# Optimization experiments

Hardware: AMD Instinct MI355X
Metric: run time of the kernel (lower is better)

## Reference

```python
import jax, jax.numpy as jnp
import numpy as np

G = 1024        # graphs in batch
NPG = 64        # nodes per graph
EPG = 256       # edges per graph
N = G * NPG     # 65536 total nodes
E = G * EPG     # 262144 total edges
IN_CH = 768
CH = 128
RATIO = 0.5
K = int(RATIO * EPG)  # edges reserved as 'causal' per graph


def setup_inputs() -> dict:
    key = jax.random.key(0)
    ks = jax.random.split(key, 10)
    w = lambda k, shape, fan: (jax.random.normal(k, shape, jnp.float32) / np.float32(np.sqrt(fan)))
    x = jax.random.normal(ks[0], (N, IN_CH), jnp.float32)
    # per-graph random edges, offset into the global node index space
    ei = jax.random.randint(ks[1], (2, G, EPG), 0, NPG)
    edge_index = (ei + (jnp.arange(G) * NPG)[None, :, None]).reshape(2, -1).astype(jnp.int32)
    edge_attr = jax.random.uniform(ks[2], (E,), jnp.float32)  # positive edge weights
    batch = jnp.repeat(jnp.arange(G, dtype=jnp.int32), NPG)
    return dict(
        x=x, edge_index=edge_index, edge_attr=edge_attr, batch=batch,
        W1=w(ks[3], (IN_CH, CH), IN_CH), V1=w(ks[4], (IN_CH, CH), IN_CH), b1=jnp.zeros((CH,), jnp.float32),
        W2=w(ks[5], (CH, CH), CH),       V2=w(ks[6], (CH, CH), CH),       b2=jnp.zeros((CH,), jnp.float32),
        mw1=w(ks[7], (2 * CH, 4 * CH), 2 * CH), mb1=jnp.zeros((4 * CH,), jnp.float32),
        mw2=w(ks[8], (4 * CH, 1), 4 * CH),      mb2=jnp.zeros((1,), jnp.float32),
    )


def reference(x, edge_index, edge_attr, batch, W1, V1, b1, W2, V2, b2, mw1, mb1, mw2, mb2):
    row, col = edge_index[0], edge_index[1]
    ew = edge_attr.reshape(-1)

    # gcn_norm (symmetric, no self loops), as used inside ARMAConv
    deg = jnp.zeros((N,), x.dtype).at[col].add(ew)
    dis = jnp.where(deg > 0, jax.lax.rsqrt(jnp.where(deg > 0, deg, 1.0)), 0.0)
    norm = dis[row] * ew * dis[col]  # [E]

    def arma(h, W, V, b):
        # ARMAConv, num_stacks=1, num_layers=1: ReLU(A_hat (h W) + h V + b)
        m = h @ W                                            # [N, C]
        agg = jnp.zeros((N, W.shape[1]), h.dtype).at[col].add(norm[:, None] * m[row])
        return jax.nn.relu(agg + h @ V + b)

    x1 = jax.nn.relu(arma(x, W1, V1, b1))  # outer F.relu (idempotent after internal ReLU)
    x2 = arma(x1, W2, V2, b2)              # [N, CH]

    # edge-gather MLP -> scalar score per edge
    edge_rep = jnp.concatenate([x2[row], x2[col]], axis=-1)          # [E, 2C]
    pred_edge_weight = (jax.nn.relu(edge_rep @ mw1 + mb1) @ mw2 + mb2).reshape(-1)  # [E]

    # per-graph top-k split (batched replacement of the numpy argpartition loop)
    wg = pred_edge_weight.reshape(G, EPG)
    order = jnp.argsort(-wg, axis=1)                                  # descending
    base = (jnp.arange(G) * EPG)[:, None]
    cid = (base + order[:, :K]).reshape(-1)   # causal (reserved) edge ids
    did = (base + order[:, K:]).reshape(-1)   # conf (dropped) edge ids

    causal = (x2, edge_index[:, cid], edge_attr[cid], pred_edge_weight[cid], batch)
    conf = (x2, edge_index[:, did], edge_attr[did], -pred_edge_weight[did], batch)
    return (*causal, *conf, pred_edge_weight)
```

## Files before the change

kernel.cpp:

```cpp
#include <hip/hip_runtime.h>
#include <hip/hip_bf16.h>
#include <stdint.h>

#define G_    1024
#define NPG   64
#define EPG   256
#define N_    (G_*NPG)
#define E_    (G_*EPG)
#define IN_CH 768
#define CH    128
#define KSEL  128
#define HID   512

#define NCH  (N_*CH)
#define GK   (G_*KSEL)
#define OFF0 0
#define OFF1 (OFF0 + NCH)
#define OFF2 (OFF1 + 2*GK)
#define OFF3 (OFF2 + GK)
#define OFF4 (OFF3 + GK)
#define OFF5 (OFF4 + N_)
#define OFF6 (OFF5 + NCH)
#define OFF7 (OFF6 + 2*GK)
#define OFF8 (OFF7 + GK)
#define OFF9 (OFF8 + GK)
#define OFF10 (OFF9 + N_)

typedef unsigned short u16;
typedef unsigned int   u32;
typedef __attribute__((ext_vector_type(8))) short bf16x8;
typedef __attribute__((ext_vector_type(4))) float f32x4;

__device__ __forceinline__ u16 f2bf(float x) {
    union { float f; u32 u; } v; v.f = x;
    u32 r = v.u + 0x7fffu + ((v.u >> 16) & 1u);
    return (u16)(r >> 16);
}
__device__ __forceinline__ float bf2f(u32 h) {
    union { u32 u; float f; } v; v.u = h << 16; return v.f;
}
__device__ __forceinline__ u16 bfc(float x) {
    __hip_bfloat16 h = __float2bfloat16(x);
    return *reinterpret_cast<u16*>(&h);
}

__global__ void k_concat(const float* __restrict__ W1, const float* __restrict__ V1,
                         const float* __restrict__ W2, const float* __restrict__ V2,
                         const float* __restrict__ mw1,
                         u16* __restrict__ WV1t, u16* __restrict__ WV2t,
                         u16* __restrict__ Mwt) {
    int i = blockIdx.x * 256 + threadIdx.x;
    if (i < 256 * IN_CH) {
        int c = i / IN_CH, r = i - c * IN_CH;
        WV1t[i] = f2bf(c < CH ? W1[r*CH + c] : V1[r*CH + (c - CH)]);
    }
    if (i < 256 * CH) {
        int c = i >> 7, r = i & 127;
        WV2t[i] = f2bf(c < CH ? W2[r*CH + c] : V2[r*CH + (c - CH)]);
    }
    if (i < 1024 * CH) {
        int c = i >> 7, r = i & 127;
        Mwt[i] = f2bf(c < HID ? mw1[r*HID + c] : mw1[(CH + r)*HID + (c - HID)]);
    }
}

__global__ __launch_bounds__(256) void k_gemm1(const float* __restrict__ Ap,
        const u16* __restrict__ Bt, u16* __restrict__ Cp) {
    __shared__ float As[2][128 * 32];
    const int t = threadIdx.x;
    const int lane = t & 63, w = t >> 6;
    const int wr = (w >> 1) << 6, wc = (w & 1) << 6;
    const size_t bm = (size_t)blockIdx.x * 128;
    const size_t bn = (size_t)blockIdx.y * 128;
    const int r16 = lane & 15, kq = lane >> 4;

    int cid[4], grow[4], gcol[4];
    #pragma unroll
    for (int i = 0; i < 4; ++i) {
        int c = i * 256 + t;
        cid[i] = c;
        int row = c >> 3, sl = c & 7;
        grow[i] = row;
        gcol[i] = (sl ^ (row & 7)) * 4;
    }

    f32x4 acc[4][4];
    #pragma unroll
    for (int m = 0; m < 4; ++m)
        #pragma unroll
        for (int n = 0; n < 4; ++n)
            acc[m][n] = (f32x4){0.f, 0.f, 0.f, 0.f};

    #define STAGE(buf, k0)                                                      \
        do {                                                                    \
            _Pragma("unroll")                                                   \
            for (int i = 0; i < 4; ++i) {                                       \
                const float* src = Ap + (bm + grow[i]) * (size_t)IN_CH + (k0) + gcol[i]; \
                __builtin_amdgcn_global_load_lds(                               \
                    (const __attribute__((address_space(1))) void*)src,         \
                    (__attribute__((address_space(3))) void*)&As[buf][cid[i] * 4], \
                    16, 0, 0);                                                  \
            }                                                                   \
        } while (0)

    #define LOADB(bv, k0)                                                       \
        do {                                                                    \
            _Pragma("unroll")                                                   \
            for (int n = 0; n < 4; ++n)                                         \
                bv[n] = *(const bf16x8*)(Bt + (bn + wc + n * 16 + r16) * (size_t)IN_CH + (k0) + kq * 8); \
        } while (0)

    STAGE(0, 0);
    bf16x8 bc[4];
    LOADB(bc, 0);
    __syncthreads();

    const int nk = IN_CH / 32;
    int buf = 0;
    for (int ki = 0; ki < nk; ++ki) {
        bf16x8 bnx[4];
        if (ki + 1 < nk) {
            STAGE(buf ^ 1, (ki + 1) * 32);
            LOADB(bnx, (ki + 1) * 32);
        }
        bf16x8 a[4];
        #pragma unroll
        for (int m = 0; m < 4; ++m) {
            int row = wr + m * 16 + r16;
            int xr = row & 7;
            const float* base = &As[buf][row * 32];
            float4 q0 = *(const float4*)(base + (((2 * kq)     ^ xr) * 4));
            float4 q1 = *(const float4*)(base + (((2 * kq + 1) ^ xr) * 4));
            union { bf16x8 v; u16 s[8]; } pk;
            pk.s[0] = bfc(q0.x); pk.s[1] = bfc(q0.y); pk.s[2] = bfc(q0.z); pk.s[3] = bfc(q0.w);
            pk.s[4] = bfc(q1.x); pk.s[5] = bfc(q1.y); pk.s[6] = bfc(q1.z); pk.s[7] = bfc(q1.w);
            a[m] = pk.v;
        }
        #pragma unroll
        for (int m = 0; m < 4; ++m)
            #pragma unroll
            for (int n = 0; n < 4; ++n)
                acc[m][n] = __builtin_amdgcn_mfma_f32_16x16x32_bf16(a[m], bc[n], acc[m][n], 0, 0, 0);
        if (ki + 1 < nk) {
            #pragma unroll
            for (int n = 0; n < 4; ++n) bc[n] = bnx[n];
        }
        __syncthreads();
        buf ^= 1;
    }
    #undef STAGE
    #undef LOADB

    #pragma unroll
    for (int m = 0; m < 4; ++m)
        #pragma unroll
        for (int j = 0; j < 4; ++j) {
            size_t row = bm + wr + m * 16 + kq * 4 + j;
            #pragma unroll
            for (int n = 0; n < 4; ++n) {
                size_t col = bn + wc + n * 16 + r16;
                Cp[row * 256 + col] = f2bf(acc[m][n][j]);
            }
        }
}

__global__ __launch_bounds__(512, 4) void k_graph(const u16* __restrict__ B1b,
        const u16* __restrict__ WV2t, const u16* __restrict__ Mwt,
        const int* __restrict__ ei,
        const float* __restrict__ b1, const float* __restrict__ b2,
        const float* __restrict__ mb1, const float* __restrict__ mw2,
        const float* __restrict__ mb2, const float* __restrict__ ea,
        float* __restrict__ out) {
    __shared__ char Lds[71168];
    float* A_s   = (float*)(Lds + 0);
    float* key   = (float*)(Lds + 0);
    u16*   x1s   = (u16*)(Lds + 16640);
    u16*   x2s   = (u16*)(Lds + 16640);
    u16*   Ms    = (u16*)(Lds + 34048);
    u16*   MVs   = (u16*)(Lds + 34048);
    u16*   PQc   = (u16*)(Lds + 34048);
    float* mw2s  = (float*)(Lds + 68864);
    float* deg_s = (float*)(Lds + 70912);

    const int g = blockIdx.x, t = threadIdx.x;
    const int lane = t & 63, w = t >> 6;
    const int r16 = lane & 15, kq = lane >> 4;
    const size_t nbase = (size_t)g * 64;
    union bfr { bf16x8 v; u16 s[8]; };

    if (t < 128) *(float4*)&mw2s[t * 4] = *(const float4*)&mw2[t * 4];
    for (int i = t; i < 64 * 65; i += 512) A_s[i] = 0.f;
    if (t < 64) deg_s[t] = 0.f;
    for (int i = t; i < 64 * 32; i += 512) {
        int row = i >> 5, c4 = (i & 31) << 2;
        *(uint2*)&Ms[row * 136 + c4] = *(const uint2*)(B1b + (nbase + row) * 256 + c4);
    }
    int rfull = 0, cfull = 0, er = 0, ec = 0; float eav = 0.f;
    if (t < 256) {
        int e = g * 256 + t;
        rfull = ei[e]; cfull = ei[E_ + e];
        er = rfull & 63; ec = cfull & 63;
        eav = ea[e];
    }
    __syncthreads();
    if (t < 256) atomicAdd(&deg_s[ec], eav);
    __syncthreads();
    if (t < 256) {
        float dr = deg_s[er], dc = deg_s[ec];
        float fr = dr > 0.f ? 1.0f / sqrtf(dr) : 0.f;
        float fc = dc > 0.f ? 1.0f / sqrtf(dc) : 0.f;
        atomicAdd(&A_s[er * 65 + ec], fr * eav * fc);
    }
    __syncthreads();

    {
        const int n0 = w * 16;
        f32x4 acc[4];
        #pragma unroll
        for (int mt = 0; mt < 4; ++mt) acc[mt] = (f32x4){0.f, 0.f, 0.f, 0.f};
        #pragma unroll
        for (int ks = 0; ks < 2; ++ks) {
            bfr a[4], b;
            #pragma unroll
            for (int mt = 0; mt < 4; ++mt)
                #pragma unroll
                for (int i = 0; i < 8; ++i)
                    a[mt].s[i] = f2bf(A_s[(ks*32 + kq*8 + i) * 65 + mt*16 + r16]);
            #pragma unroll
            for (int i = 0; i < 8; ++i)
                b.s[i] = Ms[(ks*32 + kq*8 + i) * 136 + n0 + r16];
            #pragma unroll
            for (int mt = 0; mt < 4; ++mt)
                acc[mt] = __builtin_amdgcn_mfma_f32_16x16x32_bf16(a[mt].v, b.v, acc[mt], 0, 0, 0);
        }
        const int ch = w * 16 + r16;
        __syncthreads();
        #pragma unroll
        for (int mt = 0; mt < 4; ++mt)
            #pragma unroll
            for (int j = 0; j < 4; ++j) {
                int c = mt * 16 + kq * 4 + j;
                float v = bf2f(B1b[(nbase + c) * 256 + 128 + ch]) + b1[ch];
                x1s[c * 136 + ch] = f2bf(fmaxf(acc[mt][j] + v, 0.f));
            }
    }
    __syncthreads();

    {
        const int wc2 = w * 32;
        f32x4 acc[4][2];
        #pragma unroll
        for (int mt = 0; mt < 4; ++mt)
            #pragma unroll
            for (int n = 0; n < 2; ++n) acc[mt][n] = (f32x4){0.f, 0.f, 0.f, 0.f};
        #pragma unroll
        for (int ks = 0; ks < 4; ++ks) {
            bf16x8 a[4], b[2];
            #pragma unroll
            for (int mt = 0; mt < 4; ++mt)
                a[mt] = *(const bf16x8*)&x1s[(mt*16 + r16) * 136 + ks*32 + kq*8];
            #pragma unroll
            for (int n = 0; n < 2; ++n)
                b[n] = *(const bf16x8*)(WV2t + (size_t)(wc2 + n*16 + r16) * 128 + ks*32 + kq*8);
            #pragma unroll
            for (int mt = 0; mt < 4; ++mt)
                #pragma unroll
                for (int n = 0; n < 2; ++n)
                    acc[mt][n] = __builtin_amdgcn_mfma_f32_16x16x32_bf16(a[mt], b[n], acc[mt][n], 0, 0, 0);
        }
        #pragma unroll
        for (int mt = 0; mt < 4; ++mt)
            #pragma unroll
            for (int j = 0; j < 4; ++j) {
                int row = mt * 16 + kq * 4 + j;
                #pragma unroll
                for (int n = 0; n < 2; ++n)
                    MVs[row * 272 + wc2 + n*16 + r16] = f2bf(acc[mt][n][j]);
            }
    }
    __syncthreads();

    {
        const int n0 = w * 16;
        f32x4 acc[4];
        #pragma unroll
        for (int mt = 0; mt < 4; ++mt) acc[mt] = (f32x4){0.f, 0.f, 0.f, 0.f};
        #pragma unroll
        for (int ks = 0; ks < 2; ++ks) {
            bfr a[4], b;
            #pragma unroll
            for (int mt = 0; mt < 4; ++mt)
                #pragma unroll
                for (int i = 0; i < 8; ++i)
                    a[mt].s[i] = f2bf(A_s[(ks*32 + kq*8 + i) * 65 + mt*16 + r16]);
            #pragma unroll
            for (int i = 0; i < 8; ++i)
                b.s[i] = MVs[(ks*32 + kq*8 + i) * 272 + n0 + r16];
            #pragma unroll
            for (int mt = 0; mt < 4; ++mt)
                acc[mt] = __builtin_amdgcn_mfma_f32_16x16x32_bf16(a[mt].v, b.v, acc[mt], 0, 0, 0);
        }
        const int ch = w * 16 + r16;
        #pragma unroll
        for (int mt = 0; mt < 4; ++mt)
            #pragma unroll
            for (int j = 0; j < 4; ++j) {
                int c = mt * 16 + kq * 4 + j;
                float v = bf2f(MVs[c * 272 + 128 + ch]) + b2[ch];
                float r = fmaxf(acc[mt][j] + v, 0.f);
                x2s[c * 136 + ch] = f2bf(r);
            }
    }
    __syncthreads();

    const int le = lane & 31, jh = lane >> 5;
    const int eloc = w * 32 + le;
    const int e_g = g * 256 + eloc;
    const int er6 = ei[e_g] & 63, ec6 = ei[E_ + e_g] & 63;
    float esum = 0.f;
    #pragma unroll 1
    for (int h = 0; h < 4; ++h) {
        const int wc5 = w * 32;
        f32x4 acc[4][2];
        #pragma unroll
        for (int mt = 0; mt < 4; ++mt)
            #pragma unroll
            for (int n = 0; n < 2; ++n) acc[mt][n] = (f32x4){0.f, 0.f, 0.f, 0.f};
        #pragma unroll
        for (int ks = 0; ks < 4; ++ks) {
            bf16x8 a[4], b[2];
            #pragma unroll
            for (int mt = 0; mt < 4; ++mt)
                a[mt] = *(const bf16x8*)&x2s[(mt*16 + r16) * 136 + ks*32 + kq*8];
            #pragma unroll
            for (int n = 0; n < 2; ++n) {
                int colc = wc5 + n * 16 + r16;
                int mwrow = (colc < 128) ? (h * 128 + colc) : (512 + h * 128 + (colc - 128));
                b[n] = *(const bf16x8*)(Mwt + (size_t)mwrow * 128 + ks*32 + kq*8);
            }
            #pragma unroll
            for (int mt = 0; mt < 4; ++mt)
                #pragma unroll
                for (int n = 0; n < 2; ++n)
                    acc[mt][n] = __builtin_amdgcn_mfma_f32_16x16x32_bf16(a[mt], b[n], acc[mt][n], 0, 0, 0);
        }
        #pragma unroll
        for (int n = 0; n < 2; ++n) {
            int colc = wc5 + n * 16 + r16;
            float bias = (colc < 128) ? mb1[h * 128 + colc] : 0.f;
            #pragma unroll
            for (int mt = 0; mt < 4; ++mt)
                #pragma unroll
                for (int j = 0; j < 4; ++j) {
                    int row = mt * 16 + kq * 4 + j;
                    PQc[row * 260 + colc] = f2bf(acc[mt][n][j] + bias);
                }
        }
        __syncthreads();
        {
            const u16* pP = &PQc[er6 * 260 + jh * 64];
            const u16* pQ = &PQc[ec6 * 260 + 128 + jh * 64];
            const float* pW = &mw2s[h * 128 + jh * 64];
            #pragma unroll
            for (int it = 0; it < 8; ++it) {
                uint4 up = *(const uint4*)(pP + it * 8);
                uint4 uq = *(const uint4*)(pQ + it * 8);
                float4 w0 = *(const float4*)(pW + it * 8);
                float4 w1 = *(const float4*)(pW + it * 8 + 4);
                u32 pu[4] = {up.x, up.y, up.z, up.w};
                u32 qu[4] = {uq.x, uq.y, uq.z, uq.w};
                float ww[8] = {w0.x,w0.y,w0.z,w0.w,w1.x,w1.y,w1.z,w1.w};
                #pragma unroll
                for (int k = 0; k < 4; ++k) {
                    float p0 = bf2f(pu[k] & 0xffffu), p1 = bf2f(pu[k] >> 16);
                    float q0 = bf2f(qu[k] & 0xffffu), q1 = bf2f(qu[k] >> 16);
                    esum += fmaxf(p0 + q0, 0.f) * ww[2*k];
                    esum += fmaxf(p1 + q1, 0.f) * ww[2*k + 1];
                }
            }
        }
        __syncthreads();
    }
    {
        float s = esum + __shfl_xor(esum, 32, 64);
        if (lane < 32) {
            float pv = s + mb2[0];
            out[OFF10 + e_g] = pv;
            key[eloc] = pv;
        }
    }
    __syncthreads();

    if (t < 256) {
        float ki = key[t];
        int rank = 0;
        const float4* k4 = (const float4*)key;
        #pragma unroll 4
        for (int j4 = 0; j4 < 64; ++j4) {
            float4 kv = k4[j4];
            int j = j4 * 4;
            rank += (kv.x > ki) || (kv.x == ki && (j + 0) < t);
            rank += (kv.y > ki) || (kv.y == ki && (j + 1) < t);
            rank += (kv.z > ki) || (kv.z == ki && (j + 2) < t);
            rank += (kv.w > ki) || (kv.w == ki && (j + 3) < t);
        }
        float r = (float)rfull;
        float c = (float)cfull;
        if (rank < KSEL) {
            int oo = g * KSEL + rank;
            out[OFF1 + oo]      = r;
            out[OFF1 + GK + oo] = c;
            out[OFF2 + oo]      = eav;
            out[OFF3 + oo]      = ki;
        } else {
            int oo = g * KSEL + (rank - KSEL);
            out[OFF6 + oo]      = r;
            out[OFF6 + GK + oo] = c;
            out[OFF7 + oo]      = eav;
            out[OFF8 + oo]      = -ki;
        }
    }

    {
        float* o0 = out + OFF0 + nbase * 128;
        float* o5 = out + OFF5 + nbase * 128;
        #pragma unroll
        for (int it = 0; it < 4; ++it) {
            int i = it * 512 + t;
            int node = i >> 5;
            int ch4 = (i << 2) & 127;
            uint2 d = *(const uint2*)&x2s[node * 136 + ch4];
            float4 v;
            v.x = bf2f(d.x & 0xffffu); v.y = bf2f(d.x >> 16);
            v.z = bf2f(d.y & 0xffffu); v.w = bf2f(d.y >> 16);
            *(float4*)(o0 + (i << 2)) = v;
            *(float4*)(o5 + (i << 2)) = v;
        }
        if (t < 64) {
            out[OFF4 + nbase + t] = (float)g;
            out[OFF9 + nbase + t] = (float)g;
        }
    }
}

extern "C" void kernel_launch(void* const* d_in, const int* in_sizes, int n_in,
                              void* d_out, int out_size, void* d_ws, size_t ws_size,
                              hipStream_t stream) {
    const float* x     = (const float*)d_in[0];
    const int*   ei    = (const int*)  d_in[1];
    const float* ea    = (const float*)d_in[2];
    const float* W1    = (const float*)d_in[4];
    const float* V1    = (const float*)d_in[5];
    const float* b1    = (const float*)d_in[6];
    const float* W2    = (const float*)d_in[7];
    const float* V2    = (const float*)d_in[8];
    const float* b2    = (const float*)d_in[9];
    const float* mw1   = (const float*)d_in[10];
    const float* mb1   = (const float*)d_in[11];
    const float* mw2   = (const float*)d_in[12];
    const float* mb2   = (const float*)d_in[13];
    float* out = (float*)d_out;

    char* ws = (char*)d_ws;
    size_t o = 0;
    u16* WV1t   = (u16*)(ws + o);   o += (size_t)256 * IN_CH * 2;
    u16* WV2t   = (u16*)(ws + o);   o += (size_t)256 * CH * 2;
    u16* Mwt    = (u16*)(ws + o);   o += (size_t)1024 * CH * 2;
    u16* B1b    = (u16*)(ws + o);   o += (size_t)N_ * 256 * 2;

    k_concat<<<768, 256, 0, stream>>>(W1, V1, W2, V2, mw1, WV1t, WV2t, Mwt);

    dim3 g1(N_/128, 2);
    k_gemm1<<<g1, 256, 0, stream>>>(x, WV1t, B1b);

    k_graph<<<G_, 512, 0, stream>>>(B1b, WV2t, Mwt, ei, b1, b2,
                                    mb1, mw2, mb2, ea, out);
}
```

Baseline: 214.6 us.

## Process two graphs per block with four waves each and wider per-wave tiles

Each 512-thread block now handles two graphs, with 256 threads (4 waves) per graph and separate LDS slices, so the launch uses half as many blocks. Every wave covers twice as many output columns in each MFMA stage, and each thread computes one whole edge score instead of splitting it across two half-lanes with a shuffle. The aim is better operand reuse per wave, no idle half-block in the edge and top-k phases, and fewer blocks. In exchange the block needs double the LDS, which may limit residency, and each wave carries more accumulator registers.

```diff
diff --git a/kernel.cpp b/kernel.cpp
--- a/kernel.cpp
+++ b/kernel.cpp
@@ -164,48 +164,50 @@
         }
 }
 
-__global__ __launch_bounds__(512, 4) void k_graph(const u16* __restrict__ B1b,
+#define SLICE 71168
+__global__ __launch_bounds__(512) void k_graph(const u16* __restrict__ B1b,
         const u16* __restrict__ WV2t, const u16* __restrict__ Mwt,
         const int* __restrict__ ei,
         const float* __restrict__ b1, const float* __restrict__ b2,
         const float* __restrict__ mb1, const float* __restrict__ mw2,
         const float* __restrict__ mb2, const float* __restrict__ ea,
         float* __restrict__ out) {
-    __shared__ char Lds[71168];
-    float* A_s   = (float*)(Lds + 0);
-    float* key   = (float*)(Lds + 0);
-    u16*   x1s   = (u16*)(Lds + 16640);
-    u16*   x2s   = (u16*)(Lds + 16640);
-    u16*   Ms    = (u16*)(Lds + 34048);
-    u16*   MVs   = (u16*)(Lds + 34048);
-    u16*   PQc   = (u16*)(Lds + 34048);
-    float* mw2s  = (float*)(Lds + 68864);
-    float* deg_s = (float*)(Lds + 70912);
-
-    const int g = blockIdx.x, t = threadIdx.x;
-    const int lane = t & 63, w = t >> 6;
+    __shared__ char Lds[2 * SLICE];
+    const int t = threadIdx.x;
+    const int half = t >> 8;
+    const int tl = t & 255;
+    char* L = Lds + half * SLICE;
+    float* A_s   = (float*)(L + 0);
+    float* key   = (float*)(L + 0);
+    u16*   x1s   = (u16*)(L + 16640);
+    u16*   x2s   = (u16*)(L + 16640);
+    u16*   Ms    = (u16*)(L + 34048);
+    u16*   MVs   = (u16*)(L + 34048);
+    u16*   PQc   = (u16*)(L + 34048);
+    float* mw2s  = (float*)(L + 68864);
+    float* deg_s = (float*)(L + 70912);
+
+    const int g = blockIdx.x * 2 + half;
+    const int lane = tl & 63, w4 = tl >> 6;
     const int r16 = lane & 15, kq = lane >> 4;
     const size_t nbase = (size_t)g * 64;
     union bfr { bf16x8 v; u16 s[8]; };
 
-    if (t < 128) *(float4*)&mw2s[t * 4] = *(const float4*)&mw2[t * 4];
-    for (int i = t; i < 64 * 65; i += 512) A_s[i] = 0.f;
-    if (t < 64) deg_s[t] = 0.f;
-    for (int i = t; i < 64 * 32; i += 512) {
+    if (tl < 128) *(float4*)&mw2s[tl * 4] = *(const float4*)&mw2[tl * 4];
+    for (int i = tl; i < 64 * 65; i += 256) A_s[i] = 0.f;
+    if (tl < 64) deg_s[tl] = 0.f;
+    for (int i = tl; i < 64 * 32; i += 256) {
         int row = i >> 5, c4 = (i & 31) << 2;
         *(uint2*)&Ms[row * 136 + c4] = *(const uint2*)(B1b + (nbase + row) * 256 + c4);
     }
-    int rfull = 0, cfull = 0, er = 0, ec = 0; float eav = 0.f;
-    if (t < 256) {
-        int e = g * 256 + t;
-        rfull = ei[e]; cfull = ei[E_ + e];
-        er = rfull & 63; ec = cfull & 63;
-        eav = ea[e];
-    }
-    __syncthreads();
-    if (t < 256) atomicAdd(&deg_s[ec], eav);
-    __syncthreads();
-    if (t < 256) {
+    const int e_g = g * 256 + tl;
+    const int rfull = ei[e_g], cfull = ei[E_ + e_g];
+    const int er = rfull & 63, ec = cfull & 63;
+    const float eav = ea[e_g];
+    __syncthreads();
+    atomicAdd(&deg_s[ec], eav);
+    __syncthreads();
+    {
         float dr = deg_s[er], dc = deg_s[ec];
         float fr = dr > 0.f ? 1.0f / sqrtf(dr) : 0.f;
         float fc = dc > 0.f ? 1.0f / sqrtf(dc) : 0.f;
@@ -214,58 +216,67 @@
     __syncthreads();
 
     {
-        const int n0 = w * 16;
-        f32x4 acc[4];
-        #pragma unroll
-        for (int mt = 0; mt < 4; ++mt) acc[mt] = (f32x4){0.f, 0.f, 0.f, 0.f};
+        const int n0 = w4 * 32;
+        f32x4 acc[4][2];
+        #pragma unroll
+        for (int mt = 0; mt < 4; ++mt)
+            #pragma unroll
+            for (int nt = 0; nt < 2; ++nt) acc[mt][nt] = (f32x4){0.f, 0.f, 0.f, 0.f};
         #pragma unroll
         for (int ks = 0; ks < 2; ++ks) {
-            bfr a[4], b;
+            bfr a[4], b[2];
             #pragma unroll
             for (int mt = 0; mt < 4; ++mt)
                 #pragma unroll
                 for (int i = 0; i < 8; ++i)
                     a[mt].s[i] = f2bf(A_s[(ks*32 + kq*8 + i) * 65 + mt*16 + r16]);
             #pragma unroll
-            for (int i = 0; i < 8; ++i)
-                b.s[i] = Ms[(ks*32 + kq*8 + i) * 136 + n0 + r16];
-            #pragma unroll
-            for (int mt = 0; mt < 4; ++mt)
-                acc[mt] = __builtin_amdgcn_mfma_f32_16x16x32_bf16(a[mt].v, b.v, acc[mt], 0, 0, 0);
-        }
-        const int ch = w * 16 + r16;
+            for (int nt = 0; nt < 2; ++nt)
+                #pragma unroll
+                for (int i = 0; i < 8; ++i)
+                    b[nt].s[i] = Ms[(ks*32 + kq*8 + i) * 136 + n0 + nt*16 + r16];
+            #pragma unroll
+            for (int mt = 0; mt < 4; ++mt)
+                #pragma unroll
+                for (int nt = 0; nt < 2; ++nt)
+                    acc[mt][nt] = __builtin_amdgcn_mfma_f32_16x16x32_bf16(a[mt].v, b[nt].v, acc[mt][nt], 0, 0, 0);
+        }
         __syncthreads();
         #pragma unroll
         for (int mt = 0; mt < 4; ++mt)
             #pragma unroll
             for (int j = 0; j < 4; ++j) {
                 int c = mt * 16 + kq * 4 + j;
-                float v = bf2f(B1b[(nbase + c) * 256 + 128 + ch]) + b1[ch];
-                x1s[c * 136 + ch] = f2bf(fmaxf(acc[mt][j] + v, 0.f));
-            }
-    }
-    __syncthreads();
-
-    {
-        const int wc2 = w * 32;
-        f32x4 acc[4][2];
-        #pragma unroll
-        for (int mt = 0; mt < 4; ++mt)
-            #pragma unroll
-            for (int n = 0; n < 2; ++n) acc[mt][n] = (f32x4){0.f, 0.f, 0.f, 0.f};
+                #pragma unroll
+                for (int nt = 0; nt < 2; ++nt) {
+                    int ch = n0 + nt * 16 + r16;
+                    float v = bf2f(B1b[(nbase + c) * 256 + 128 + ch]) + b1[ch];
+                    x1s[c * 136 + ch] = f2bf(fmaxf(acc[mt][nt][j] + v, 0.f));
+                }
+            }
+    }
+    __syncthreads();
+
+    {
+        const int wc2 = w4 * 64;
+        f32x4 acc[4][4];
+        #pragma unroll
+        for (int mt = 0; mt < 4; ++mt)
+            #pragma unroll
+            for (int n = 0; n < 4; ++n) acc[mt][n] = (f32x4){0.f, 0.f, 0.f, 0.f};
         #pragma unroll
         for (int ks = 0; ks < 4; ++ks) {
-            bf16x8 a[4], b[2];
+            bf16x8 a[4], b[4];
             #pragma unroll
             for (int mt = 0; mt < 4; ++mt)
                 a[mt] = *(const bf16x8*)&x1s[(mt*16 + r16) * 136 + ks*32 + kq*8];
             #pragma unroll
-            for (int n = 0; n < 2; ++n)
+            for (int n = 0; n < 4; ++n)
                 b[n] = *(const bf16x8*)(WV2t + (size_t)(wc2 + n*16 + r16) * 128 + ks*32 + kq*8);
             #pragma unroll
             for (int mt = 0; mt < 4; ++mt)
                 #pragma unroll
-                for (int n = 0; n < 2; ++n)
+                for (int n = 0; n < 4; ++n)
                     acc[mt][n] = __builtin_amdgcn_mfma_f32_16x16x32_bf16(a[mt], b[n], acc[mt][n], 0, 0, 0);
         }
         #pragma unroll
@@ -274,66 +285,70 @@
             for (int j = 0; j < 4; ++j) {
                 int row = mt * 16 + kq * 4 + j;
                 #pragma unroll
-                for (int n = 0; n < 2; ++n)
+                for (int n = 0; n < 4; ++n)
                     MVs[row * 272 + wc2 + n*16 + r16] = f2bf(acc[mt][n][j]);
             }
     }
     __syncthreads();
 
     {
-        const int n0 = w * 16;
-        f32x4 acc[4];
-        #pragma unroll
-        for (int mt = 0; mt < 4; ++mt) acc[mt] = (f32x4){0.f, 0.f, 0.f, 0.f};
+        const int n0 = w4 * 32;
+        f32x4 acc[4][2];
+        #pragma unroll
+        for (int mt = 0; mt < 4; ++mt)
+            #pragma unroll
+            for (int nt = 0; nt < 2; ++nt) acc[mt][nt] = (f32x4){0.f, 0.f, 0.f, 0.f};
         #pragma unroll
         for (int ks = 0; ks < 2; ++ks) {
-            bfr a[4], b;
+            bfr a[4], b[2];
             #pragma unroll
             for (int mt = 0; mt < 4; ++mt)
                 #pragma unroll
                 for (int i = 0; i < 8; ++i)
                     a[mt].s[i] = f2bf(A_s[(ks*32 + kq*8 + i) * 65 + mt*16 + r16]);
             #pragma unroll
-            for (int i = 0; i < 8; ++i)
-                b.s[i] = MVs[(ks*32 + kq*8 + i) * 272 + n0 + r16];
-            #pragma unroll
-            for (int mt = 0; mt < 4; ++mt)
-                acc[mt] = __builtin_amdgcn_mfma_f32_16x16x32_bf16(a[mt].v, b.v, acc[mt], 0, 0, 0);
-        }
-        const int ch = w * 16 + r16;
+            for (int nt = 0; nt < 2; ++nt)
+                #pragma unroll
+                for (int i = 0; i < 8; ++i)
+                    b[nt].s[i] = MVs[(ks*32 + kq*8 + i) * 272 + n0 + nt*16 + r16];
+            #pragma unroll
+            for (int mt = 0; mt < 4; ++mt)
+                #pragma unroll
+                for (int nt = 0; nt < 2; ++nt)
+                    acc[mt][nt] = __builtin_amdgcn_mfma_f32_16x16x32_bf16(a[mt].v, b[nt].v, acc[mt][nt], 0, 0, 0);
+        }
         #pragma unroll
         for (int mt = 0; mt < 4; ++mt)
             #pragma unroll
             for (int j = 0; j < 4; ++j) {
                 int c = mt * 16 + kq * 4 + j;
-                float v = bf2f(MVs[c * 272 + 128 + ch]) + b2[ch];
-                float r = fmaxf(acc[mt][j] + v, 0.f);
-                x2s[c * 136 + ch] = f2bf(r);
-            }
-    }
-    __syncthreads();
-
-    const int le = lane & 31, jh = lane >> 5;
-    const int eloc = w * 32 + le;
-    const int e_g = g * 256 + eloc;
-    const int er6 = ei[e_g] & 63, ec6 = ei[E_ + e_g] & 63;
+                #pragma unroll
+                for (int nt = 0; nt < 2; ++nt) {
+                    int ch = n0 + nt * 16 + r16;
+                    float v = bf2f(MVs[c * 272 + 128 + ch]) + b2[ch];
+                    x2s[c * 136 + ch] = f2bf(fmaxf(acc[mt][nt][j] + v, 0.f));
+                }
+            }
+    }
+    __syncthreads();
+
     float esum = 0.f;
     #pragma unroll 1
     for (int h = 0; h < 4; ++h) {
-        const int wc5 = w * 32;
-        f32x4 acc[4][2];
-        #pragma unroll
-        for (int mt = 0; mt < 4; ++mt)
-            #pragma unroll
-            for (int n = 0; n < 2; ++n) acc[mt][n] = (f32x4){0.f, 0.f, 0.f, 0.f};
+        const int wc5 = w4 * 64;
+        f32x4 acc[4][4];
+        #pragma unroll
+        for (int mt = 0; mt < 4; ++mt)
+            #pragma unroll
+            for (int n = 0; n < 4; ++n) acc[mt][n] = (f32x4){0.f, 0.f, 0.f, 0.f};
         #pragma unroll
         for (int ks = 0; ks < 4; ++ks) {
-            bf16x8 a[4], b[2];
+            bf16x8 a[4], b[4];
             #pragma unroll
             for (int mt = 0; mt < 4; ++mt)
                 a[mt] = *(const bf16x8*)&x2s[(mt*16 + r16) * 136 + ks*32 + kq*8];
             #pragma unroll
-            for (int n = 0; n < 2; ++n) {
+            for (int n = 0; n < 4; ++n) {
                 int colc = wc5 + n * 16 + r16;
                 int mwrow = (colc < 128) ? (h * 128 + colc) : (512 + h * 128 + (colc - 128));
                 b[n] = *(const bf16x8*)(Mwt + (size_t)mwrow * 128 + ks*32 + kq*8);
@@ -341,11 +356,11 @@
             #pragma unroll
             for (int mt = 0; mt < 4; ++mt)
                 #pragma unroll
-                for (int n = 0; n < 2; ++n)
+                for (int n = 0; n < 4; ++n)
                     acc[mt][n] = __builtin_amdgcn_mfma_f32_16x16x32_bf16(a[mt], b[n], acc[mt][n], 0, 0, 0);
         }
         #pragma unroll
-        for (int n = 0; n < 2; ++n) {
+        for (int n = 0; n < 4; ++n) {
             int colc = wc5 + n * 16 + r16;
             float bias = (colc < 128) ? mb1[h * 128 + colc] : 0.f;
             #pragma unroll
@@ -358,11 +373,11 @@
         }
         __syncthreads();
         {
-            const u16* pP = &PQc[er6 * 260 + jh * 64];
-            const u16* pQ = &PQc[ec6 * 260 + 128 + jh * 64];
-            const float* pW = &mw2s[h * 128 + jh * 64];
-            #pragma unroll
-            for (int it = 0; it < 8; ++it) {
+            const u16* pP = &PQc[er * 260];
+            const u16* pQ = &PQc[ec * 260 + 128];
+            const float* pW = &mw2s[h * 128];
+            #pragma unroll
+            for (int it = 0; it < 16; ++it) {
                 uint4 up = *(const uint4*)(pP + it * 8);
                 uint4 uq = *(const uint4*)(pQ + it * 8);
                 float4 w0 = *(const float4*)(pW + it * 8);
@@ -381,28 +396,22 @@
         }
         __syncthreads();
     }
-    {
-        float s = esum + __shfl_xor(esum, 32, 64);
-        if (lane < 32) {
-            float pv = s + mb2[0];
-            out[OFF10 + e_g] = pv;
-            key[eloc] = pv;
-        }
-    }
-    __syncthreads();
-
-    if (t < 256) {
-        float ki = key[t];
+    const float pv = esum + mb2[0];
+    out[OFF10 + e_g] = pv;
+    key[tl] = pv;
+    __syncthreads();
+
+    {
         int rank = 0;
         const float4* k4 = (const float4*)key;
         #pragma unroll 4
         for (int j4 = 0; j4 < 64; ++j4) {
             float4 kv = k4[j4];
             int j = j4 * 4;
-            rank += (kv.x > ki) || (kv.x == ki && (j + 0) < t);
-            rank += (kv.y > ki) || (kv.y == ki && (j + 1) < t);
-            rank += (kv.z > ki) || (kv.z == ki && (j + 2) < t);
-            rank += (kv.w > ki) || (kv.w == ki && (j + 3) < t);
+            rank += (kv.x > pv) || (kv.x == pv && (j + 0) < tl);
+            rank += (kv.y > pv) || (kv.y == pv && (j + 1) < tl);
+            rank += (kv.z > pv) || (kv.z == pv && (j + 2) < tl);
+            rank += (kv.w > pv) || (kv.w == pv && (j + 3) < tl);
         }
         float r = (float)rfull;
         float c = (float)cfull;
@@ -411,13 +420,13 @@
             out[OFF1 + oo]      = r;
             out[OFF1 + GK + oo] = c;
             out[OFF2 + oo]      = eav;
-            out[OFF3 + oo]      = ki;
+            out[OFF3 + oo]      = pv;
         } else {
             int oo = g * KSEL + (rank - KSEL);
             out[OFF6 + oo]      = r;
             out[OFF6 + GK + oo] = c;
             out[OFF7 + oo]      = eav;
-            out[OFF8 + oo]      = -ki;
+            out[OFF8 + oo]      = -pv;
         }
     }
 
@@ -425,8 +434,8 @@
         float* o0 = out + OFF0 + nbase * 128;
         float* o5 = out + OFF5 + nbase * 128;
         #pragma unroll
-        for (int it = 0; it < 4; ++it) {
-            int i = it * 512 + t;
+        for (int it = 0; it < 8; ++it) {
+            int i = it * 256 + tl;
             int node = i >> 5;
             int ch4 = (i << 2) & 127;
             uint2 d = *(const uint2*)&x2s[node * 136 + ch4];
@@ -436,9 +445,9 @@
             *(float4*)(o0 + (i << 2)) = v;
             *(float4*)(o5 + (i << 2)) = v;
         }
-        if (t < 64) {
-            out[OFF4 + nbase + t] = (float)g;
-            out[OFF9 + nbase + t] = (float)g;
+        if (tl < 64) {
+            out[OFF4 + nbase + tl] = (float)g;
+            out[OFF9 + nbase + tl] = (float)g;
         }
     }
 }
@@ -473,6 +482,6 @@
     dim3 g1(N_/128, 2);
     k_gemm1<<<g1, 256, 0, stream>>>(x, WV1t, B1b);
 
-    k_graph<<<G_, 512, 0, stream>>>(B1b, WV2t, Mwt, ei, b1, b2,
-                                    mb1, mw2, mb2, ea, out);
-}
+    k_graph<<<G_/2, 512, 0, stream>>>(B1b, WV2t, Mwt, ei, b1, b2,
+                                      mb1, mw2, mb2, ea, out);
+}
```

After: 238.8 us. 11.3% more time.
